# Kernel optimization log

Measured on AMD Instinct MI355X. Metric: run time of the kernel, lower is better.

The kernel has to match this reference:

```python
import jax, jax.numpy as jnp
import numpy as np

# (dv=3, dc=6)-regular Tanner graph: M checks, N=2M vars, E=M*dc edges
M, N, DV, DC, D, B, T = 1024, 2048, 3, 6, 8, 128, 5
CIN = DC * D          # check-MLP in/out dim = 48
VIN = DV * D + 1      # var-MLP in/out dim  = 25 (extra scalar = LLR)
HC, HV = 4 * CIN, 4 * VIN
EPS = 1e-6


def _graph():
    # variable j connects to checks (j + l) % M, l = 0..DV-1 -> every check has degree DC
    var_nbrs = (np.arange(N)[:, None] + np.arange(DV)[None, :]) % M   # [N, DV] check ids
    # var-edge id e = j*DV + l ; sort edges by check to get check-slot ordering
    order = np.argsort(var_nbrs.reshape(-1), kind='stable')           # check-edge p -> var-edge e
    chk_nbrs = (order // DV).reshape(M, DC)                           # var id in each check slot
    inv_order = np.argsort(order)                                     # var-edge e -> check-edge p
    return chk_nbrs, order, inv_order


def setup_inputs() -> dict:
    key = jax.random.key(0)
    ks = jax.random.split(key, 12)
    chk_nbrs, order, inv_order = _graph()
    prior = np.clip(np.random.default_rng(0).uniform(0.005, 0.05, size=N), EPS, 1 - EPS)
    prior_llr = jnp.asarray(np.log((1.0 - prior) / prior), jnp.float32)

    def lin_w(k, g, nin, nout):
        return jax.random.normal(k, (g, nin, nout), jnp.float32) / np.sqrt(nin)

    def lin_b(k, g, nout):
        return 0.02 * jax.random.normal(k, (g, nout), jnp.float32)

    return {
        "syndromes": jax.random.randint(ks[0], (B, M), 0, 2, jnp.int32),
        "prior_llr": prior_llr,
        "chk_w1": lin_w(ks[1], M, CIN, HC), "chk_b1": lin_b(ks[2], M, HC),
        "chk_w2": lin_w(ks[3], M, HC, CIN), "chk_b2": lin_b(ks[4], M, CIN),
        "var_w1": lin_w(ks[5], N, VIN, HV), "var_b1": lin_b(ks[6], N, HV),
        "var_w2": lin_w(ks[7], N, HV, VIN), "var_b2": lin_b(ks[8], N, VIN),
        "chk_nbrs": jnp.asarray(chk_nbrs, jnp.int32),      # [M, DC] var id per check slot
        "c2v_gather": jnp.asarray(inv_order, jnp.int32),   # var-edge -> check-edge perm
        "v2c_gather": jnp.asarray(order, jnp.int32),       # check-edge -> var-edge perm
    }


def reference(syndromes, prior_llr, chk_w1, chk_b1, chk_w2, chk_b2,
              var_w1, var_b1, var_w2, var_b2, chk_nbrs, c2v_gather, v2c_gather):
    synd_sgn = (1 - 2 * syndromes).astype(jnp.float32)                    # [B, M]
    prior_b = jnp.broadcast_to(prior_llr, (B, N))[..., None]              # [B, N, 1]

    def chk_mlp(x):  # x: [B, M, CIN], per-check grouped GEMM
        h = jax.nn.gelu(jnp.einsum('bmi,mih->bmh', x, chk_w1) + chk_b1, approximate=False)
        return jnp.einsum('bmh,mho->bmo', h, chk_w2) + chk_b2

    def var_mlp(x):  # x: [B, N, VIN]
        h = jax.nn.gelu(jnp.einsum('bni,nih->bnh', x, var_w1) + var_b1, approximate=False)
        return jnp.einsum('bnh,nho->bno', h, var_w2) + var_b2

    # init check in-messages: zeros with first component = prior LLR of neighbor var
    chk_in = jnp.zeros((B, M, DC, D), jnp.float32).at[..., 0].set(prior_llr[chk_nbrs][None])

    def step(chk_in, _):
        y = chk_mlp(chk_in.reshape(B, M, CIN)).reshape(B, M, DC, D)
        y = y * synd_sgn[:, :, None, None]                                # syndrome sign flip
        var_in = y.reshape(B, M * DC, D)[:, c2v_gather]                   # scatter c->v as gather
        x = jnp.concatenate([var_in.reshape(B, N, DV * D), prior_b], axis=-1)
        out = var_mlp(x)
        llr = out[..., DV * D]                                            # [B, N]
        msg = out[..., :DV * D].reshape(B, N * DV, D)
        chk_in_new = msg[:, v2c_gather].reshape(B, M, DC, D)              # scatter v->c as gather
        return chk_in_new, llr

    _, llrs = jax.lax.scan(step, chk_in, None, length=T)
    return llrs  # [T, B, N]
```

## Files before the change

### kernel.cpp

```cpp
#include <hip/hip_runtime.h>
#include <math.h>

#define MM 1024
#define NN 2048
#define BB 128
#define TT 5
#define EE 6144

typedef __bf16 bf16x8 __attribute__((ext_vector_type(8)));
typedef __bf16 bf16x4 __attribute__((ext_vector_type(4)));
typedef short  s16x4  __attribute__((ext_vector_type(4)));
typedef float  f32x4  __attribute__((ext_vector_type(4)));
typedef unsigned int u32x4 __attribute__((ext_vector_type(4)));

#define CHK_W_ELEMS 22272
#define CHK_L2_OFF  12288
#define VAR_W_ELEMS 7168
#define VAR_L2_OFF  3584

__device__ __forceinline__ float gelu_fast(float x) {
    float xe = x * 0.70710678118654752f;
    float ax = fabsf(xe);
    float t  = __builtin_amdgcn_rcpf(1.0f + 0.3275911f * ax);
    float p  = t * (0.254829592f + t * (-0.284496736f + t * (1.421413741f +
               t * (-1.453152027f + t * 1.061405429f))));
    float er = 1.0f - p * __expf(-xe * xe);
    er = copysignf(er, xe);
    return 0.5f * x * (1.0f + er);
}

__device__ __forceinline__ f32x4 mfma16(bf16x4 a, bf16x4 b, f32x4 c) {
#if __has_builtin(__builtin_amdgcn_mfma_f32_16x16x16bf16_1k)
    return __builtin_amdgcn_mfma_f32_16x16x16bf16_1k(
        __builtin_bit_cast(s16x4, a), __builtin_bit_cast(s16x4, b), c, 0, 0, 0);
#else
    f32x4 d;
    asm volatile("v_mfma_f32_16x16x16_bf16 %0, %1, %2, %3\n\ts_nop 4"
                 : "=v"(d) : "v"(a), "v"(b), "v"(c));
    return d;
#endif
}

__device__ __forceinline__ void wave_lds_fence() {
    asm volatile("s_waitcnt lgkmcnt(0)" ::: "memory");
}

#define PREP_GRID (1024 + 2048 + 512 + 3072)

__global__ __launch_bounds__(256)
void prep_fused(const float* __restrict__ cw1, const float* __restrict__ cb1,
                const float* __restrict__ cw2, const float* __restrict__ cb2,
                const float* __restrict__ vw1, const float* __restrict__ vb1,
                const float* __restrict__ vw2, const float* __restrict__ vb2,
                const int* __restrict__ synd, const float* __restrict__ prior,
                __bf16* __restrict__ wchk, __bf16* __restrict__ wvar,
                float* __restrict__ sgnT, __bf16* __restrict__ v2c)
{
    const int bid = blockIdx.x;
    const int tid = threadIdx.x;

    __shared__ __align__(16) float s[18672];

    if (bid < 1024) {
        const int m = bid;
        {
            const float4* g1 = (const float4*)(cw1 + (size_t)m * 9216);
            const float4* g2 = (const float4*)(cw2 + (size_t)m * 9216);
            float4* s4 = (float4*)s;
            #pragma unroll
            for (int it = 0; it < 9; ++it) s4[it * 256 + tid] = g1[it * 256 + tid];
            #pragma unroll
            for (int it = 0; it < 9; ++it) s4[2304 + it * 256 + tid] = g2[it * 256 + tid];
            if (tid < 192) s[18432 + tid] = cb1[(size_t)m * 192 + tid];
            if (tid < 48)  s[18624 + tid] = cb2[(size_t)m * 48 + tid];
        }
        __syncthreads();

        __bf16* dst = wchk + (size_t)m * CHK_W_ELEMS;

        #pragma unroll
        for (int it = 0; it < 6; ++it) {
            int i = it * 256 + tid;
            int l = i & 63, f = i >> 6;
            int mt = f >> 1, kt = f & 1, q = l >> 4, c = l & 15;
            int h = mt * 16 + c;
            bf16x8 v;
            #pragma unroll
            for (int j = 0; j < 8; ++j) {
                int k  = kt * 32 + q * 8 + j;
                int kc = min(k, 47);
                float wv = s[kc * 192 + h];
                float x  = (k < 48) ? wv : ((k == 48) ? s[18432 + h] : 0.0f);
                v[j] = (__bf16)x;
            }
            *(bf16x8*)(dst + i * 8) = v;
        }
        #pragma unroll
        for (int it = 0; it < 10; ++it) {
            int i = it * 256 + tid;
            if (i < 2496) {
                int l = i & 63, f = i >> 6;
                int ks = f / 3, mt = f - ks * 3;
                int q = l >> 4, c = l & 15, o = mt * 16 + c;
                bf16x4 v;
                #pragma unroll
                for (int r = 0; r < 4; ++r) {
                    int k  = ks * 16 + q * 4 + r;
                    int kc = min(k, 191);
                    float wv = s[9216 + kc * 48 + o];
                    float x  = (k < 192) ? wv : ((k == 192) ? s[18624 + o] : 0.0f);
                    v[r] = (__bf16)x;
                }
                *(bf16x4*)(dst + CHK_L2_OFF + i * 4) = v;
            }
        }
    } else if (bid < 3072) {
        const int nv = bid - 1024;
        {
            const float4* g1 = (const float4*)(vw1 + (size_t)nv * 2500);
            const float4* g2 = (const float4*)(vw2 + (size_t)nv * 2500);
            float4* s4 = (float4*)s;
            #pragma unroll
            for (int it = 0; it < 3; ++it) {
                int i = it * 256 + tid;
                if (i < 625) s4[i] = g1[i];
            }
            #pragma unroll
            for (int it = 0; it < 3; ++it) {
                int i = it * 256 + tid;
                if (i < 625) s4[625 + i] = g2[i];
            }
            if (tid < 100) s[5000 + tid] = vb1[(size_t)nv * 100 + tid];
            if (tid < 25)  s[5100 + tid] = vb2[(size_t)nv * 25 + tid];
        }
        __syncthreads();

        __bf16* dst = wvar + (size_t)nv * VAR_W_ELEMS;

        #pragma unroll
        for (int it = 0; it < 2; ++it) {
            int i = it * 256 + tid;
            if (i < 448) {
                int l = i & 63, mt = i >> 6;
                int q = l >> 4, c = l & 15, h = mt * 16 + c;
                int hc = min(h, 99);
                bf16x8 v;
                #pragma unroll
                for (int j = 0; j < 8; ++j) {
                    int k  = q * 8 + j;
                    int kc = min(k, 24);
                    float wv = s[kc * 100 + hc];
                    float x = 0.0f;
                    if (h < 100) x = (k < 25) ? wv : ((k == 25) ? s[5000 + h] : 0.0f);
                    v[j] = (__bf16)x;
                }
                *(bf16x8*)(dst + i * 8) = v;
            }
        }
        #pragma unroll
        for (int it = 0; it < 4; ++it) {
            int i = it * 256 + tid;
            if (i < 896) {
                int l = i & 63, f = i >> 6;
                int ks = f >> 1, mt = f & 1;
                int q = l >> 4, c = l & 15, o = mt * 16 + c;
                int oc = min(o, 24);
                bf16x4 v;
                #pragma unroll
                for (int r = 0; r < 4; ++r) {
                    int k  = ks * 16 + q * 4 + r;
                    int kc = min(k, 99);
                    float wv = s[2500 + kc * 25 + oc];
                    float x = 0.0f;
                    if (o < 25) x = (k < 100) ? wv : ((k == 100) ? s[5100 + o] : 0.0f);
                    v[r] = (__bf16)x;
                }
                *(bf16x4*)(dst + VAR_L2_OFF + i * 4) = v;
            }
        }
    } else if (bid < 3584) {
        int idx = (bid - 3072) * 256 + tid;
        int m = idx >> 7, b = idx & 127;
        sgnT[idx] = (float)(1 - 2 * synd[(size_t)b * MM + m]);
    } else {
        int idx = (bid - 3584) * 256 + tid;
        int e = idx >> 7;
        bf16x8 v;
        #pragma unroll
        for (int j = 0; j < 8; ++j) v[j] = (__bf16)0.0f;
        v[0] = (__bf16)prior[e / 3];
        *(bf16x8*)(v2c + (size_t)idx * 8) = v;
    }
}

#define CPITCH 58
__global__ __launch_bounds__(256, 3)
void chk_kernel(const __bf16* __restrict__ wchk,
                const float* __restrict__ sgnT,
                const int* __restrict__ v2c_gather,
                const __bf16* __restrict__ v2c, __bf16* __restrict__ c2v)
{
    const int m = blockIdx.x;
    const int tid = threadIdx.x;
    const int w = tid >> 6, l = tid & 63, q = l >> 4, c = l & 15;

    __shared__ __align__(16) __bf16 wlds[CHK_W_ELEMS];
    __shared__ __align__(16) __bf16 ytile[4 * 16 * CPITCH];
    {
        const __bf16* src = wchk + (size_t)m * CHK_W_ELEMS;
        for (int i = tid; i < CHK_W_ELEMS / 8; i += 256)
            *(u32x4*)(wlds + i * 8) = *(const u32x4*)(src + i * 8);
    }
    const int e0 = v2c_gather[m * 6 + q];
    const int e1 = (q < 2) ? v2c_gather[m * 6 + 4 + q] : 0;
    __syncthreads();

    __bf16* myy = ytile + w * 16 * CPITCH;

    for (int t2 = 0; t2 < 2; ++t2) {
        const int bt = t2 * 64 + w * 16;

        bf16x8 b0 = *(const bf16x8*)(v2c + ((size_t)e0 * BB + bt + c) * 8);
        bf16x8 b1f;
        #pragma unroll
        for (int j = 0; j < 8; ++j) b1f[j] = (__bf16)0.0f;
        if (q < 2)       b1f = *(const bf16x8*)(v2c + ((size_t)e1 * BB + bt + c) * 8);
        else if (q == 2) b1f[0] = (__bf16)1.0f;

        f32x4 acc[12];
        #pragma unroll
        for (int mt = 0; mt < 12; ++mt) {
            bf16x8 a0 = *(const bf16x8*)(wlds + (mt * 2 + 0) * 512 + l * 8);
            bf16x8 a1 = *(const bf16x8*)(wlds + (mt * 2 + 1) * 512 + l * 8);
            f32x4 z = {0.f, 0.f, 0.f, 0.f};
            z = __builtin_amdgcn_mfma_f32_16x16x32_bf16(a0, b0, z, 0, 0, 0);
            z = __builtin_amdgcn_mfma_f32_16x16x32_bf16(a1, b1f, z, 0, 0, 0);
            acc[mt] = z;
        }

        f32x4 acc2[3];
        #pragma unroll
        for (int mt = 0; mt < 3; ++mt) acc2[mt] = (f32x4){0.f, 0.f, 0.f, 0.f};
        #pragma unroll
        for (int ks = 0; ks < 13; ++ks) {
            bf16x4 bf;
            if (ks < 12) {
                #pragma unroll
                for (int r = 0; r < 4; ++r) bf[r] = (__bf16)gelu_fast(acc[ks][r]);
            } else {
                #pragma unroll
                for (int r = 0; r < 4; ++r) bf[r] = (__bf16)0.0f;
                if (q == 0) bf[0] = (__bf16)1.0f;
            }
            #pragma unroll
            for (int mt = 0; mt < 3; ++mt) {
                bf16x4 af = *(const bf16x4*)(wlds + CHK_L2_OFF + (ks * 3 + mt) * 256 + l * 4);
                acc2[mt] = mfma16(af, bf, acc2[mt]);
            }
        }

        const float sg = sgnT[m * BB + bt + c];
        #pragma unroll
        for (int mt = 0; mt < 3; ++mt)
            #pragma unroll
            for (int r = 0; r < 4; ++r)
                myy[c * CPITCH + mt * 16 + q * 4 + r] = (__bf16)(acc2[mt][r] * sg);
        wave_lds_fence();

        {
            int s = l >> 4, row = l & 15;
            u32x4 vv = *(const u32x4*)(myy + row * CPITCH + s * 8);
            *(u32x4*)(c2v + ((size_t)(m * 6 + s) * BB + bt + row) * 8) = vv;
            if (l < 32) {
                int s2 = 4 + (l >> 4), row2 = l & 15;
                u32x4 v2 = *(const u32x4*)(myy + row2 * CPITCH + s2 * 8);
                *(u32x4*)(c2v + ((size_t)(m * 6 + s2) * BB + bt + row2) * 8) = v2;
            }
        }
        wave_lds_fence();
    }
}

#define VPITCH 26
__global__ __launch_bounds__(256, 4)
void var_kernel(const __bf16* __restrict__ wvar,
                const int* __restrict__ c2v_gather, const float* __restrict__ prior,
                const __bf16* __restrict__ c2v, __bf16* __restrict__ v2c,
                float* __restrict__ llr_out, int last)
{
    const int nv = blockIdx.x;
    const int tid = threadIdx.x;
    const int w = tid >> 6, l = tid & 63, q = l >> 4, c = l & 15;

    __shared__ __align__(16) __bf16 wlds[VAR_W_ELEMS];
    __shared__ __align__(16) __bf16 ytile[4 * 16 * VPITCH];
    {
        const __bf16* src = wvar + (size_t)nv * VAR_W_ELEMS;
        for (int i = tid; i < VAR_W_ELEMS / 8; i += 256)
            *(u32x4*)(wlds + i * 8) = *(const u32x4*)(src + i * 8);
    }
    const int ep = (q < 3) ? c2v_gather[nv * 3 + q] : 0;
    const __bf16 prbf = (__bf16)prior[nv];
    __syncthreads();

    __bf16* myy = ytile + w * 16 * VPITCH;

    for (int t2 = 0; t2 < 2; ++t2) {
        const int bt = t2 * 64 + w * 16;

        bf16x8 b0;
        #pragma unroll
        for (int j = 0; j < 8; ++j) b0[j] = (__bf16)0.0f;
        if (q < 3) b0 = *(const bf16x8*)(c2v + ((size_t)ep * BB + bt + c) * 8);
        else { b0[0] = prbf; b0[1] = (__bf16)1.0f; }

        f32x4 acc[7];
        #pragma unroll
        for (int mt = 0; mt < 7; ++mt) {
            bf16x8 a0 = *(const bf16x8*)(wlds + mt * 512 + l * 8);
            f32x4 z = {0.f, 0.f, 0.f, 0.f};
            acc[mt] = __builtin_amdgcn_mfma_f32_16x16x32_bf16(a0, b0, z, 0, 0, 0);
        }

        f32x4 acc2[2];
        acc2[0] = (f32x4){0.f, 0.f, 0.f, 0.f};
        acc2[1] = (f32x4){0.f, 0.f, 0.f, 0.f};
        #pragma unroll
        for (int ks = 0; ks < 7; ++ks) {
            bf16x4 bf;
            #pragma unroll
            for (int r = 0; r < 4; ++r) bf[r] = (__bf16)gelu_fast(acc[ks][r]);
            if (ks == 6 && q == 1) bf[0] = (__bf16)1.0f;
            #pragma unroll
            for (int mt = 0; mt < 2; ++mt) {
                bf16x4 af = *(const bf16x4*)(wlds + VAR_L2_OFF + (ks * 2 + mt) * 256 + l * 4);
                acc2[mt] = mfma16(af, bf, acc2[mt]);
            }
        }

        #pragma unroll
        for (int r = 0; r < 4; ++r)
            myy[c * VPITCH + q * 4 + r] = (__bf16)acc2[0][r];
        if (q < 2)
            #pragma unroll
            for (int r = 0; r < 4; ++r)
                myy[c * VPITCH + 16 + q * 4 + r] = (__bf16)acc2[1][r];
        if (q == 2) llr_out[(size_t)(bt + c) * NN + nv] = acc2[1][0];
        wave_lds_fence();

        if (!last && l < 48) {
            int s = l >> 4, row = l & 15;
            u32x4 vv = *(const u32x4*)(myy + row * VPITCH + s * 8);
            *(u32x4*)(v2c + ((size_t)(nv * 3 + s) * BB + bt + row) * 8) = vv;
        }
        wave_lds_fence();
    }
}

extern "C" void kernel_launch(void* const* d_in, const int* in_sizes, int n_in,
                              void* d_out, int out_size, void* d_ws, size_t ws_size,
                              hipStream_t stream) {
    const int*   syndromes = (const int*)  d_in[0];
    const float* prior_llr = (const float*)d_in[1];
    const float* chk_w1    = (const float*)d_in[2];
    const float* chk_b1    = (const float*)d_in[3];
    const float* chk_w2    = (const float*)d_in[4];
    const float* chk_b2    = (const float*)d_in[5];
    const float* var_w1    = (const float*)d_in[6];
    const float* var_b1    = (const float*)d_in[7];
    const float* var_w2    = (const float*)d_in[8];
    const float* var_b2    = (const float*)d_in[9];
    const int*   c2v_g     = (const int*)  d_in[11];
    const int*   v2c_g     = (const int*)  d_in[12];

    float* out = (float*)d_out;

    __bf16* v2c  = (__bf16*)d_ws;
    __bf16* c2v  = v2c + (size_t)EE * BB * 8;
    __bf16* wchk = c2v + (size_t)EE * BB * 8;
    __bf16* wvar = wchk + (size_t)MM * CHK_W_ELEMS;
    float*  sgnT = (float*)(wvar + (size_t)NN * VAR_W_ELEMS);

    prep_fused<<<PREP_GRID, 256, 0, stream>>>(chk_w1, chk_b1, chk_w2, chk_b2,
                                              var_w1, var_b1, var_w2, var_b2,
                                              syndromes, prior_llr,
                                              wchk, wvar, sgnT, v2c);

    for (int t = 0; t < TT; ++t) {
        chk_kernel<<<MM, 256, 0, stream>>>(wchk, sgnT, v2c_g, v2c, c2v);
        var_kernel<<<NN, 256, 0, stream>>>(wvar, c2v_g, prior_llr, c2v, v2c,
                                           out + (size_t)t * BB * NN,
                                           (t == TT - 1) ? 1 : 0);
    }
}
```

Measured before the change: 424.0 us.

## Stream check weights through smaller LDS chunks in prep kernel to raise occupancy

The weight-prep kernel used to stage both full check-MLP weight matrices (about 73KB) in shared memory at once. It now stages them in four smaller chunks of at most 24KB, repacking each chunk to bf16 before loading the next. It also adds a launch bound hint of 6 blocks per CU. The aim is to let more blocks sit on each CU so the load-heavy prep work hides latency better. The cost is extra __syncthreads barriers and serialized load/repack phases within each block.

```diff
diff --git a/kernel.cpp b/kernel.cpp
--- a/kernel.cpp
+++ b/kernel.cpp
@@ -47,7 +47,7 @@
 
 #define PREP_GRID (1024 + 2048 + 512 + 3072)
 
-__global__ __launch_bounds__(256)
+__global__ __launch_bounds__(256, 6)
 void prep_fused(const float* __restrict__ cw1, const float* __restrict__ cb1,
                 const float* __restrict__ cw2, const float* __restrict__ cb2,
                 const float* __restrict__ vw1, const float* __restrict__ vb1,
@@ -58,97 +58,124 @@
 {
     const int bid = blockIdx.x;
     const int tid = threadIdx.x;
-
-    __shared__ __align__(16) float s[18672];
+    const int w = tid >> 6, l = tid & 63, q = l >> 4, c = l & 15;
+
+    __shared__ __align__(16) float s[6144];
+    float4* s4 = (float4*)s;
 
     if (bid < 1024) {
         const int m = bid;
-        {
-            const float4* g1 = (const float4*)(cw1 + (size_t)m * 9216);
-            const float4* g2 = (const float4*)(cw2 + (size_t)m * 9216);
-            float4* s4 = (float4*)s;
-            #pragma unroll
-            for (int it = 0; it < 9; ++it) s4[it * 256 + tid] = g1[it * 256 + tid];
-            #pragma unroll
-            for (int it = 0; it < 9; ++it) s4[2304 + it * 256 + tid] = g2[it * 256 + tid];
-            if (tid < 192) s[18432 + tid] = cb1[(size_t)m * 192 + tid];
-            if (tid < 48)  s[18624 + tid] = cb2[(size_t)m * 48 + tid];
-        }
-        __syncthreads();
-
+        const float4* g1 = (const float4*)(cw1 + (size_t)m * 9216);
+        const float4* g2 = (const float4*)(cw2 + (size_t)m * 9216);
         __bf16* dst = wchk + (size_t)m * CHK_W_ELEMS;
 
         #pragma unroll
-        for (int it = 0; it < 6; ++it) {
-            int i = it * 256 + tid;
-            int l = i & 63, f = i >> 6;
-            int mt = f >> 1, kt = f & 1, q = l >> 4, c = l & 15;
+        for (int it = 0; it < 6; ++it) s4[it * 256 + tid] = g1[it * 256 + tid];
+        __syncthreads();
+        #pragma unroll
+        for (int it = 0; it < 3; ++it) {
+            int mt = it * 4 + w;
             int h = mt * 16 + c;
             bf16x8 v;
             #pragma unroll
+            for (int j = 0; j < 8; ++j) v[j] = (__bf16)s[(q * 8 + j) * 192 + h];
+            *(bf16x8*)(dst + (mt * 2) * 512 + l * 8) = v;
+        }
+        __syncthreads();
+
+        #pragma unroll
+        for (int it = 0; it < 3; ++it) s4[it * 256 + tid] = g1[1536 + it * 256 + tid];
+        if (tid < 192) s[3072 + tid] = cb1[(size_t)m * 192 + tid];
+        __syncthreads();
+        #pragma unroll
+        for (int it = 0; it < 3; ++it) {
+            int mt = it * 4 + w;
+            int h = mt * 16 + c;
+            bf16x8 v;
+            #pragma unroll
             for (int j = 0; j < 8; ++j) {
-                int k  = kt * 32 + q * 8 + j;
-                int kc = min(k, 47);
-                float wv = s[kc * 192 + h];
-                float x  = (k < 48) ? wv : ((k == 48) ? s[18432 + h] : 0.0f);
-                v[j] = (__bf16)x;
-            }
-            *(bf16x8*)(dst + i * 8) = v;
-        }
-        #pragma unroll
-        for (int it = 0; it < 10; ++it) {
+                int lr = q * 8 + j;
+                float wv = s[lr * 192 + h];
+                v[j] = (__bf16)((lr <= 16) ? wv : 0.0f);
+            }
+            *(bf16x8*)(dst + (mt * 2 + 1) * 512 + l * 8) = v;
+        }
+        __syncthreads();
+
+        #pragma unroll
+        for (int it = 0; it < 5; ++it) {
             int i = it * 256 + tid;
-            if (i < 2496) {
-                int l = i & 63, f = i >> 6;
-                int ks = f / 3, mt = f - ks * 3;
-                int q = l >> 4, c = l & 15, o = mt * 16 + c;
+            if (i < 1152) s4[i] = g2[i];
+        }
+        __syncthreads();
+        #pragma unroll
+        for (int it = 0; it < 5; ++it) {
+            int fl = it * 4 + w;
+            if (fl < 18) {
+                int ks = fl / 3, mt = fl % 3;
+                int o = mt * 16 + c;
                 bf16x4 v;
                 #pragma unroll
+                for (int r = 0; r < 4; ++r)
+                    v[r] = (__bf16)s[(ks * 16 + q * 4 + r) * 48 + o];
+                *(bf16x4*)(dst + CHK_L2_OFF + fl * 256 + l * 4) = v;
+            }
+        }
+        __syncthreads();
+
+        #pragma unroll
+        for (int it = 0; it < 5; ++it) {
+            int i = it * 256 + tid;
+            if (i < 1152) s4[i] = g2[1152 + i];
+        }
+        if (tid < 48) s[4608 + tid] = cb2[(size_t)m * 48 + tid];
+        __syncthreads();
+        #pragma unroll
+        for (int it = 0; it < 6; ++it) {
+            int fl = it * 4 + w;
+            if (fl < 21) {
+                int ks6 = fl / 3, mt = fl % 3;
+                int o = mt * 16 + c;
+                bf16x4 v;
+                #pragma unroll
                 for (int r = 0; r < 4; ++r) {
-                    int k  = ks * 16 + q * 4 + r;
-                    int kc = min(k, 191);
-                    float wv = s[9216 + kc * 48 + o];
-                    float x  = (k < 192) ? wv : ((k == 192) ? s[18624 + o] : 0.0f);
-                    v[r] = (__bf16)x;
+                    int lr = ks6 * 16 + q * 4 + r;
+                    float wv = s[lr * 48 + o];
+                    v[r] = (__bf16)((lr <= 96) ? wv : 0.0f);
                 }
-                *(bf16x4*)(dst + CHK_L2_OFF + i * 4) = v;
+                *(bf16x4*)(dst + CHK_L2_OFF + (18 + fl) * 256 + l * 4) = v;
             }
         }
     } else if (bid < 3072) {
         const int nv = bid - 1024;
-        {
-            const float4* g1 = (const float4*)(vw1 + (size_t)nv * 2500);
-            const float4* g2 = (const float4*)(vw2 + (size_t)nv * 2500);
-            float4* s4 = (float4*)s;
-            #pragma unroll
-            for (int it = 0; it < 3; ++it) {
+        const float4* g1 = (const float4*)(vw1 + (size_t)nv * 2500);
+        const float4* g2 = (const float4*)(vw2 + (size_t)nv * 2500);
+        __bf16* dst = wvar + (size_t)nv * VAR_W_ELEMS;
+
+        #pragma unroll
+        for (int it = 0; it < 3; ++it) {
+            int i = it * 256 + tid;
+            if (i < 625) s4[i] = g1[i];
+        }
+        #pragma unroll
+        for (int it = 0; it < 3; ++it) {
+            int i = it * 256 + tid;
+            if (i < 625) s4[625 + i] = g2[i];
+        }
+        if (tid < 100) s[5000 + tid] = vb1[(size_t)nv * 100 + tid];
+        if (tid < 25)  s[5100 + tid] = vb2[(size_t)nv * 25 + tid];
+        __syncthreads();
+
+        #pragma unroll
+        for (int it = 0; it < 2; ++it) {
+            int mt = it * 4 + w;
+            if (mt < 7) {
                 int i = it * 256 + tid;
-                if (i < 625) s4[i] = g1[i];
-            }
-            #pragma unroll
-            for (int it = 0; it < 3; ++it) {
-                int i = it * 256 + tid;
-                if (i < 625) s4[625 + i] = g2[i];
-            }
-            if (tid < 100) s[5000 + tid] = vb1[(size_t)nv * 100 + tid];
-            if (tid < 25)  s[5100 + tid] = vb2[(size_t)nv * 25 + tid];
-        }
-        __syncthreads();
-
-        __bf16* dst = wvar + (size_t)nv * VAR_W_ELEMS;
-
-        #pragma unroll
-        for (int it = 0; it < 2; ++it) {
-            int i = it * 256 + tid;
-            if (i < 448) {
-                int l = i & 63, mt = i >> 6;
-                int q = l >> 4, c = l & 15, h = mt * 16 + c;
-                int hc = min(h, 99);
+                int h = mt * 16 + c, hc = min(h, 99);
                 bf16x8 v;
                 #pragma unroll
                 for (int j = 0; j < 8; ++j) {
-                    int k  = q * 8 + j;
-                    int kc = min(k, 24);
+                    int k = q * 8 + j, kc = min(k, 24);
                     float wv = s[kc * 100 + hc];
                     float x = 0.0f;
                     if (h < 100) x = (k < 25) ? wv : ((k == 25) ? s[5000 + h] : 0.0f);
@@ -159,17 +186,15 @@
         }
         #pragma unroll
         for (int it = 0; it < 4; ++it) {
-            int i = it * 256 + tid;
-            if (i < 896) {
-                int l = i & 63, f = i >> 6;
-                int ks = f >> 1, mt = f & 1;
-                int q = l >> 4, c = l & 15, o = mt * 16 + c;
-                int oc = min(o, 24);
+            int fl = it * 4 + w;
+            if (fl < 14) {
+                int i = it * 256 + tid;
+                int ks = fl >> 1, mt = fl & 1;
+                int o = mt * 16 + c, oc = min(o, 24);
                 bf16x4 v;
                 #pragma unroll
                 for (int r = 0; r < 4; ++r) {
-                    int k  = ks * 16 + q * 4 + r;
-                    int kc = min(k, 99);
+                    int k = ks * 16 + q * 4 + r, kc = min(k, 99);
                     float wv = s[2500 + kc * 25 + oc];
                     float x = 0.0f;
                     if (o < 25) x = (k < 100) ? wv : ((k == 100) ? s[5100 + o] : 0.0f);
```

Result: faster. 403.5 us (-4.8%).
